# Kernel tuning notes

Hardware: AMD Instinct MI355X
Metric: run time of the kernel (lower is better)

## Reference

```python
import jax, jax.numpy as jnp
import numpy as np

# Each of the 16 binary logic gates, relaxed to real values, is a multilinear
# function: gate(a,b) = c0 + c1*a + c2*b + c3*a*b. Rows follow the standard
# difflogic ordering: FALSE, AND, a&~b, a, ~a&b, b, XOR, OR, NOR, XNOR,
# ~b, a|~b, ~a, ~a|b, NAND, TRUE.
GATE_COEF = jnp.array([
    [0.0,  0.0,  0.0,  0.0],   # 0:  false
    [0.0,  0.0,  0.0,  1.0],   # 1:  a AND b
    [0.0,  1.0,  0.0, -1.0],   # 2:  a AND NOT b
    [0.0,  1.0,  0.0,  0.0],   # 3:  a
    [0.0,  0.0,  1.0, -1.0],   # 4:  NOT a AND b
    [0.0,  0.0,  1.0,  0.0],   # 5:  b
    [0.0,  1.0,  1.0, -2.0],   # 6:  a XOR b
    [0.0,  1.0,  1.0, -1.0],   # 7:  a OR b
    [1.0, -1.0, -1.0,  1.0],   # 8:  NOR
    [1.0, -1.0, -1.0,  2.0],   # 9:  XNOR
    [1.0,  0.0, -1.0,  0.0],   # 10: NOT b
    [1.0,  0.0, -1.0,  1.0],   # 11: a OR NOT b
    [1.0, -1.0,  0.0,  0.0],   # 12: NOT a
    [1.0, -1.0,  0.0,  1.0],   # 13: NOT a OR b
    [1.0,  0.0,  0.0, -1.0],   # 14: NAND
    [1.0,  0.0,  0.0,  0.0],   # 15: true
], dtype=jnp.float32)

B, IN_DIM, HIDDEN, N_LAYERS, OUT_DIM, TAU = 4096, 1024, 8192, 6, 8, 10.0
NPO = HIDDEN // OUT_DIM  # neurons_per_output


def logic_layer(h, w, ia, ib):
    # h: [B, in_dim]; w: [H, 16]; ia, ib: [H] int indices into in_dim.
    # Softmax-weighted blend of 16 gates == multilinear form with blended coefs.
    p = jax.nn.softmax(w, axis=-1)          # [H, 16]
    c = p @ GATE_COEF                       # [H, 4]
    a = h[:, ia]                            # [B, H] gather
    b = h[:, ib]                            # [B, H] gather
    return c[:, 0] + c[:, 1] * a + c[:, 2] * b + c[:, 3] * (a * b)


def setup_inputs() -> dict:
    key = jax.random.key(0)
    ks = jax.random.split(key, 8)
    return {
        "x": jax.random.uniform(ks[0], (B, IN_DIM), dtype=jnp.float32),
        "logic_w": jax.random.normal(ks[1], (N_LAYERS, HIDDEN, 16), dtype=jnp.float32),
        "scaler_w": jax.random.normal(ks[2], (OUT_DIM, OUT_DIM), dtype=jnp.float32) * 0.1,
        "scaler_b": jax.random.normal(ks[3], (OUT_DIM,), dtype=jnp.float32) * 0.1,
        "idx0_a": jax.random.randint(ks[4], (HIDDEN,), 0, IN_DIM, dtype=jnp.int32),
        "idx0_b": jax.random.randint(ks[5], (HIDDEN,), 0, IN_DIM, dtype=jnp.int32),
        "idx_a": jax.random.randint(ks[6], (N_LAYERS - 1, HIDDEN), 0, HIDDEN, dtype=jnp.int32),
        "idx_b": jax.random.randint(ks[7], (N_LAYERS - 1, HIDDEN), 0, HIDDEN, dtype=jnp.int32),
    }


def reference(x, logic_w, scaler_w, scaler_b, idx0_a, idx0_b, idx_a, idx_b):
    h = (x.reshape(x.shape[0], -1) > 0.5).astype(jnp.float32)   # binarize
    h = logic_layer(h, logic_w[0], idx0_a, idx0_b)               # [B, HIDDEN]
    for i in range(N_LAYERS - 1):
        h = logic_layer(h, logic_w[i + 1], idx_a[i], idx_b[i])
    h = h.reshape(h.shape[0], OUT_DIM, NPO)                      # [B, O, NPO]
    values = jnp.sum(h, axis=2) / TAU                            # [B, O]
    q_values = values @ scaler_w.T + scaler_b                    # nn.Linear
    return q_values
```

## Files before the change

### kernel.cpp

```cpp
#include <hip/hip_runtime.h>
#include <hip/hip_fp16.h>

constexpr int BATCH    = 4096;
constexpr int IN_DIM   = 1024;
constexpr int HIDDEN   = 8192;
constexpr int N_LAYERS = 6;
constexpr int N_STAGES = N_LAYERS / 2;
constexpr int OUT_DIM  = 8;
constexpr float INV_TAU = 0.1f;

constexpr int TB   = 8;
constexpr int NTH  = 1024;
constexpr int NPT  = HIDDEN / NTH;
constexpr int NWAVES = NTH / 64;

__device__ __forceinline__ __half2 u2h(unsigned int u) {
    union { unsigned int u; __half2 h; } v; v.u = u; return v.h;
}
__device__ __forceinline__ unsigned int h2u(__half2 h) {
    union { unsigned int u; __half2 h; } v; v.h = h; return v.u;
}

__device__ __forceinline__ uint2 pack4(float4 v) {
    __half2 lo = __float22half2_rn(make_float2(v.x, v.y));
    __half2 hi = __float22half2_rn(make_float2(v.z, v.w));
    uint2 r; r.x = h2u(lo); r.y = h2u(hi); return r;
}

__global__ void prep_coef(const float* __restrict__ logic_w,
                          uint2* __restrict__ coefs, int n)
{
    int id = blockIdx.x * blockDim.x + threadIdx.x;
    if (id >= n) return;

    const float4* w4 = (const float4*)(logic_w + (size_t)id * 16);
    float4 wa = w4[0], wb = w4[1], wc = w4[2], wd = w4[3];
    float wv[16] = {wa.x, wa.y, wa.z, wa.w, wb.x, wb.y, wb.z, wb.w,
                    wc.x, wc.y, wc.z, wc.w, wd.x, wd.y, wd.z, wd.w};
    float m = wv[0];
#pragma unroll
    for (int i = 1; i < 16; ++i) m = fmaxf(m, wv[i]);
    float e[16];
    float s = 0.f;
#pragma unroll
    for (int i = 0; i < 16; ++i) { e[i] = expf(wv[i] - m); s += e[i]; }
    float inv = 1.f / s;
    const float G0[16] = {0,0,0,0,0,0,0,0, 1,1,1,1,1,1,1,1};
    const float G1[16] = {0,0,1,1,0,0,1,1, -1,-1,0,0,-1,-1,0,0};
    const float G2[16] = {0,0,0,0,1,1,1,1, -1,-1,-1,-1,0,0,0,0};
    const float G3[16] = {0,1,-1,0,-1,0,-2,-1, 1,2,0,1,0,1,-1,0};
    float c0 = 0.f, c1 = 0.f, c2 = 0.f, c3 = 0.f;
#pragma unroll
    for (int i = 0; i < 16; ++i) {
        float pv = e[i] * inv;
        c0 = fmaf(pv, G0[i], c0);
        c1 = fmaf(pv, G1[i], c1);
        c2 = fmaf(pv, G2[i], c2);
        c3 = fmaf(pv, G3[i], c3);
    }
    coefs[id] = pack4(make_float4(c0, c1, c2, c3));
}

__global__ void prep_fuse(const uint2* __restrict__ coefs,
                          const int* __restrict__ idx0_a,
                          const int* __restrict__ idx0_b,
                          const int* __restrict__ idx_a,
                          const int* __restrict__ idx_b,
                          uint4* __restrict__ cABp,
                          uint2* __restrict__ idx4p,
                          uint2* __restrict__ cCp, int n)
{
    int id = blockIdx.x * blockDim.x + threadIdx.x;
    if (id >= n) return;
    const int s = id >> 13;
    const int j = id & (HIDDEN - 1);
    const int ltop = 2 * s + 1;
    const int lbot = 2 * s;

    const int pa = idx_a[(size_t)(ltop - 1) * HIDDEN + j];
    const int pb = idx_b[(size_t)(ltop - 1) * HIDDEN + j];

    int gaa, gba, gab, gbb;
    if (s == 0) {
        gaa = idx0_a[pa]; gba = idx0_b[pa];
        gab = idx0_a[pb]; gbb = idx0_b[pb];
    } else {
        const int* A  = idx_a + (size_t)(lbot - 1) * HIDDEN;
        const int* Bv = idx_b + (size_t)(lbot - 1) * HIDDEN;
        gaa = A[pa]; gba = Bv[pa];
        gab = A[pb]; gbb = Bv[pb];
    }
    idx4p[id] = make_uint2((unsigned)gaa | ((unsigned)gba << 16),
                           (unsigned)gab | ((unsigned)gbb << 16));

    uint2 cA = coefs[(size_t)lbot * HIDDEN + pa];
    uint2 cB = coefs[(size_t)lbot * HIDDEN + pb];
    cABp[id] = make_uint4(cA.x, cA.y, cB.x, cB.y);
    cCp[id]  = coefs[(size_t)ltop * HIDDEN + j];
}

__device__ __forceinline__ uint4 gate8(uint4 a, uint4 b, uint2 c) {
    __half2 cp01 = u2h(c.x), cp23 = u2h(c.y);
    __half2 c0 = __low2half2(cp01), c1 = __high2half2(cp01);
    __half2 c2 = __low2half2(cp23), c3 = __high2half2(cp23);
    uint4 r;
    {
        __half2 av = u2h(a.x), bv = u2h(b.x);
        r.x = h2u(__hfma2(bv, __hfma2(c3, av, c2), __hfma2(c1, av, c0)));
    }
    {
        __half2 av = u2h(a.y), bv = u2h(b.y);
        r.y = h2u(__hfma2(bv, __hfma2(c3, av, c2), __hfma2(c1, av, c0)));
    }
    {
        __half2 av = u2h(a.z), bv = u2h(b.z);
        r.z = h2u(__hfma2(bv, __hfma2(c3, av, c2), __hfma2(c1, av, c0)));
    }
    {
        __half2 av = u2h(a.w), bv = u2h(b.w);
        r.w = h2u(__hfma2(bv, __hfma2(c3, av, c2), __hfma2(c1, av, c0)));
    }
    return r;
}

__global__ __launch_bounds__(NTH) void net_kernel(
    const float*  __restrict__ x,
    const uint4*  __restrict__ cABp,
    const uint2*  __restrict__ idx4p,
    const uint2*  __restrict__ cCp,
    const float*  __restrict__ scaler_w, const float* __restrict__ scaler_b,
    float* __restrict__ out)
{
    __shared__ uint4 h[HIDDEN];
    __shared__ uint4 hx[IN_DIM];
    __shared__ float warr[NWAVES][TB];
    __shared__ float vals[TB][OUT_DIM];

    const int tid = threadIdx.x;
    const int b0  = blockIdx.x * TB;

    {
        float v[TB];
#pragma unroll
        for (int r = 0; r < TB; ++r)
            v[r] = (x[(size_t)(b0 + r) * IN_DIM + tid] > 0.5f) ? 1.f : 0.f;
        uint4 p;
        p.x = h2u(__floats2half2_rn(v[0], v[1]));
        p.y = h2u(__floats2half2_rn(v[2], v[3]));
        p.z = h2u(__floats2half2_rn(v[4], v[5]));
        p.w = h2u(__floats2half2_rn(v[6], v[7]));
        hx[tid] = p;
    }

    uint2 ij[NPT], ijn[NPT];
    uint4 acc[NPT];

#pragma unroll
    for (int k = 0; k < NPT; ++k) ij[k] = idx4p[k * NTH + tid];

    __syncthreads();

#pragma unroll
    for (int k = 0; k < NPT; ++k) ijn[k] = idx4p[HIDDEN + k * NTH + tid];
#pragma unroll
    for (int k = 0; k < NPT; ++k) {
        uint2 p = ij[k];
        uint4 x1 = hx[p.x & 0xffffu], x2 = hx[p.x >> 16];
        uint4 x3 = hx[p.y & 0xffffu], x4 = hx[p.y >> 16];
        uint4 cab = cABp[k * NTH + tid];
        uint2 cc  = cCp[k * NTH + tid];
        uint4 u = gate8(x1, x2, make_uint2(cab.x, cab.y));
        uint4 v = gate8(x3, x4, make_uint2(cab.z, cab.w));
        acc[k] = gate8(u, v, cc);
    }
#pragma unroll
    for (int k = 0; k < NPT; ++k) h[k * NTH + tid] = acc[k];
    __syncthreads();

#pragma unroll
    for (int s = 1; s < N_STAGES; ++s) {
#pragma unroll
        for (int k = 0; k < NPT; ++k) ij[k] = ijn[k];
        if (s < N_STAGES - 1) {
#pragma unroll
            for (int k = 0; k < NPT; ++k)
                ijn[k] = idx4p[(size_t)(s + 1) * HIDDEN + k * NTH + tid];
        }
#pragma unroll
        for (int k = 0; k < NPT; ++k) {
            uint2 p = ij[k];
            uint4 x1 = h[p.x & 0xffffu], x2 = h[p.x >> 16];
            uint4 x3 = h[p.y & 0xffffu], x4 = h[p.y >> 16];
            uint4 cab = cABp[(size_t)s * HIDDEN + k * NTH + tid];
            uint2 cc  = cCp[(size_t)s * HIDDEN + k * NTH + tid];
            uint4 u = gate8(x1, x2, make_uint2(cab.x, cab.y));
            uint4 v = gate8(x3, x4, make_uint2(cab.z, cab.w));
            acc[k] = gate8(u, v, cc);
        }
        __syncthreads();
#pragma unroll
        for (int k = 0; k < NPT; ++k) h[k * NTH + tid] = acc[k];
        __syncthreads();
    }

    {
        const int k    = tid >> 7;
        const int base = k * 1024 + (tid & 127);
        float s[TB] = {0.f, 0.f, 0.f, 0.f, 0.f, 0.f, 0.f, 0.f};
#pragma unroll
        for (int i = 0; i < 8; ++i) {
            uint4 t = h[base + 128 * i];
            float2 f0 = __half22float2(u2h(t.x));
            float2 f1 = __half22float2(u2h(t.y));
            float2 f2 = __half22float2(u2h(t.z));
            float2 f3 = __half22float2(u2h(t.w));
            s[0] += f0.x; s[1] += f0.y; s[2] += f1.x; s[3] += f1.y;
            s[4] += f2.x; s[5] += f2.y; s[6] += f3.x; s[7] += f3.y;
        }
#pragma unroll
        for (int off = 32; off > 0; off >>= 1) {
#pragma unroll
            for (int r = 0; r < TB; ++r) s[r] += __shfl_down(s[r], off);
        }
        if ((tid & 63) == 0) {
#pragma unroll
            for (int r = 0; r < TB; ++r) warr[tid >> 6][r] = s[r];
        }
    }
    __syncthreads();
    if (tid < TB * OUT_DIM) {
        int r = tid >> 3;
        int k = tid & 7;
        vals[r][k] = (warr[2 * k][r] + warr[2 * k + 1][r]) * INV_TAU;
    }
    __syncthreads();
    if (tid < TB * OUT_DIM) {
        int r = tid >> 3;
        int o = tid & 7;
        float q = scaler_b[o];
#pragma unroll
        for (int k = 0; k < OUT_DIM; ++k)
            q = fmaf(vals[r][k], scaler_w[o * OUT_DIM + k], q);
        out[(size_t)(b0 + r) * OUT_DIM + o] = q;
    }
}

extern "C" void kernel_launch(void* const* d_in, const int* in_sizes, int n_in,
                              void* d_out, int out_size, void* d_ws, size_t ws_size,
                              hipStream_t stream)
{
    const float* x        = (const float*)d_in[0];
    const float* logic_w  = (const float*)d_in[1];
    const float* scaler_w = (const float*)d_in[2];
    const float* scaler_b = (const float*)d_in[3];
    const int*   idx0_a   = (const int*)d_in[4];
    const int*   idx0_b   = (const int*)d_in[5];
    const int*   idx_a    = (const int*)d_in[6];
    const int*   idx_b    = (const int*)d_in[7];
    float* out = (float*)d_out;

    const int nc = N_LAYERS * HIDDEN;
    const int nf = N_STAGES * HIDDEN;
    char* ws = (char*)d_ws;
    uint2* coefs = (uint2*)ws;                                   ws += (size_t)nc * sizeof(uint2);
    uint4* cABp  = (uint4*)ws;                                   ws += (size_t)nf * sizeof(uint4);
    uint2* idx4p = (uint2*)ws;                                   ws += (size_t)nf * sizeof(uint2);
    uint2* cCp   = (uint2*)ws;

    prep_coef<<<(nc + 255) / 256, 256, 0, stream>>>(logic_w, coefs, nc);
    prep_fuse<<<(nf + 255) / 256, 256, 0, stream>>>(coefs, idx0_a, idx0_b,
                                                    idx_a, idx_b, cABp, idx4p, cCp, nf);
    net_kernel<<<BATCH / TB, NTH, 0, stream>>>(x, cABp, idx4p, cCp,
                                               scaler_w, scaler_b, out);
}
```

Baseline: 115.8 us.

## Process two batch tiles per block and prefetch next tile's inputs

Each block now loops over two 8-row batch tiles instead of one, halving the grid size. The next tile's x values are loaded during the current tile's stage 1 and binarized into the hx buffer after stage 1, which hides the global read latency. The goal is to amortize block launch and setup cost and overlap input loads with compute. The trade-off is fewer blocks in flight (256 blocks of 1024 threads), which may leave CUs underused, plus extra registers for the prefetched values.

```diff
diff --git a/kernel.cpp b/kernel.cpp
--- a/kernel.cpp
+++ b/kernel.cpp
@@ -9,9 +9,10 @@
 constexpr int OUT_DIM  = 8;
 constexpr float INV_TAU = 0.1f;
 
-constexpr int TB   = 8;
-constexpr int NTH  = 1024;
-constexpr int NPT  = HIDDEN / NTH;
+constexpr int TB     = 8;
+constexpr int NTILES = 2;
+constexpr int NTH    = 1024;
+constexpr int NPT    = HIDDEN / NTH;
 constexpr int NWAVES = NTH / 64;
 
 __device__ __forceinline__ __half2 u2h(unsigned int u) {
@@ -137,7 +138,7 @@
     __shared__ float vals[TB][OUT_DIM];
 
     const int tid = threadIdx.x;
-    const int b0  = blockIdx.x * TB;
+    const int b0  = blockIdx.x * (TB * NTILES);
 
     {
         float v[TB];
@@ -161,87 +162,117 @@
     __syncthreads();
 
 #pragma unroll
-    for (int k = 0; k < NPT; ++k) ijn[k] = idx4p[HIDDEN + k * NTH + tid];
-#pragma unroll
-    for (int k = 0; k < NPT; ++k) {
-        uint2 p = ij[k];
-        uint4 x1 = hx[p.x & 0xffffu], x2 = hx[p.x >> 16];
-        uint4 x3 = hx[p.y & 0xffffu], x4 = hx[p.y >> 16];
-        uint4 cab = cABp[k * NTH + tid];
-        uint2 cc  = cCp[k * NTH + tid];
-        uint4 u = gate8(x1, x2, make_uint2(cab.x, cab.y));
-        uint4 v = gate8(x3, x4, make_uint2(cab.z, cab.w));
-        acc[k] = gate8(u, v, cc);
-    }
-#pragma unroll
-    for (int k = 0; k < NPT; ++k) h[k * NTH + tid] = acc[k];
-    __syncthreads();
-
-#pragma unroll
-    for (int s = 1; s < N_STAGES; ++s) {
-#pragma unroll
-        for (int k = 0; k < NPT; ++k) ij[k] = ijn[k];
-        if (s < N_STAGES - 1) {
-#pragma unroll
-            for (int k = 0; k < NPT; ++k)
-                ijn[k] = idx4p[(size_t)(s + 1) * HIDDEN + k * NTH + tid];
-        }
+    for (int t = 0; t < NTILES; ++t) {
+        const int bt = b0 + t * TB;
+        float xn[TB];
+
+#pragma unroll
+        for (int k = 0; k < NPT; ++k) ijn[k] = idx4p[HIDDEN + k * NTH + tid];
 #pragma unroll
         for (int k = 0; k < NPT; ++k) {
             uint2 p = ij[k];
-            uint4 x1 = h[p.x & 0xffffu], x2 = h[p.x >> 16];
-            uint4 x3 = h[p.y & 0xffffu], x4 = h[p.y >> 16];
-            uint4 cab = cABp[(size_t)s * HIDDEN + k * NTH + tid];
-            uint2 cc  = cCp[(size_t)s * HIDDEN + k * NTH + tid];
+            uint4 x1 = hx[p.x & 0xffffu], x2 = hx[p.x >> 16];
+            uint4 x3 = hx[p.y & 0xffffu], x4 = hx[p.y >> 16];
+            uint4 cab = cABp[k * NTH + tid];
+            uint2 cc  = cCp[k * NTH + tid];
             uint4 u = gate8(x1, x2, make_uint2(cab.x, cab.y));
             uint4 v = gate8(x3, x4, make_uint2(cab.z, cab.w));
             acc[k] = gate8(u, v, cc);
         }
-        __syncthreads();
 #pragma unroll
         for (int k = 0; k < NPT; ++k) h[k * NTH + tid] = acc[k];
         __syncthreads();
-    }
-
-    {
-        const int k    = tid >> 7;
-        const int base = k * 1024 + (tid & 127);
-        float s[TB] = {0.f, 0.f, 0.f, 0.f, 0.f, 0.f, 0.f, 0.f};
-#pragma unroll
-        for (int i = 0; i < 8; ++i) {
-            uint4 t = h[base + 128 * i];
-            float2 f0 = __half22float2(u2h(t.x));
-            float2 f1 = __half22float2(u2h(t.y));
-            float2 f2 = __half22float2(u2h(t.z));
-            float2 f3 = __half22float2(u2h(t.w));
-            s[0] += f0.x; s[1] += f0.y; s[2] += f1.x; s[3] += f1.y;
-            s[4] += f2.x; s[5] += f2.y; s[6] += f3.x; s[7] += f3.y;
-        }
-#pragma unroll
-        for (int off = 32; off > 0; off >>= 1) {
-#pragma unroll
-            for (int r = 0; r < TB; ++r) s[r] += __shfl_down(s[r], off);
-        }
-        if ((tid & 63) == 0) {
-#pragma unroll
-            for (int r = 0; r < TB; ++r) warr[tid >> 6][r] = s[r];
-        }
-    }
-    __syncthreads();
-    if (tid < TB * OUT_DIM) {
-        int r = tid >> 3;
-        int k = tid & 7;
-        vals[r][k] = (warr[2 * k][r] + warr[2 * k + 1][r]) * INV_TAU;
-    }
-    __syncthreads();
-    if (tid < TB * OUT_DIM) {
-        int r = tid >> 3;
-        int o = tid & 7;
-        float q = scaler_b[o];
-#pragma unroll
-        for (int k = 0; k < OUT_DIM; ++k)
-            q = fmaf(vals[r][k], scaler_w[o * OUT_DIM + k], q);
-        out[(size_t)(b0 + r) * OUT_DIM + o] = q;
+
+        if (t + 1 < NTILES) {
+#pragma unroll
+            for (int r = 0; r < TB; ++r)
+                xn[r] = x[(size_t)(bt + TB + r) * IN_DIM + tid];
+        }
+
+#pragma unroll
+        for (int s = 1; s < N_STAGES; ++s) {
+#pragma unroll
+            for (int k = 0; k < NPT; ++k) ij[k] = ijn[k];
+            if (s < N_STAGES - 1) {
+#pragma unroll
+                for (int k = 0; k < NPT; ++k)
+                    ijn[k] = idx4p[(size_t)(s + 1) * HIDDEN + k * NTH + tid];
+            }
+#pragma unroll
+            for (int k = 0; k < NPT; ++k) {
+                uint2 p = ij[k];
+                uint4 x1 = h[p.x & 0xffffu], x2 = h[p.x >> 16];
+                uint4 x3 = h[p.y & 0xffffu], x4 = h[p.y >> 16];
+                uint4 cab = cABp[(size_t)s * HIDDEN + k * NTH + tid];
+                uint2 cc  = cCp[(size_t)s * HIDDEN + k * NTH + tid];
+                uint4 u = gate8(x1, x2, make_uint2(cab.x, cab.y));
+                uint4 v = gate8(x3, x4, make_uint2(cab.z, cab.w));
+                acc[k] = gate8(u, v, cc);
+            }
+            __syncthreads();
+#pragma unroll
+            for (int k = 0; k < NPT; ++k) h[k * NTH + tid] = acc[k];
+            __syncthreads();
+
+            if (s == 1 && t + 1 < NTILES) {
+                uint4 p;
+                p.x = h2u(__floats2half2_rn(xn[0] > 0.5f ? 1.f : 0.f,
+                                            xn[1] > 0.5f ? 1.f : 0.f));
+                p.y = h2u(__floats2half2_rn(xn[2] > 0.5f ? 1.f : 0.f,
+                                            xn[3] > 0.5f ? 1.f : 0.f));
+                p.z = h2u(__floats2half2_rn(xn[4] > 0.5f ? 1.f : 0.f,
+                                            xn[5] > 0.5f ? 1.f : 0.f));
+                p.w = h2u(__floats2half2_rn(xn[6] > 0.5f ? 1.f : 0.f,
+                                            xn[7] > 0.5f ? 1.f : 0.f));
+                hx[tid] = p;
+            }
+        }
+
+        {
+            const int k    = tid >> 7;
+            const int base = k * 1024 + (tid & 127);
+            float s[TB] = {0.f, 0.f, 0.f, 0.f, 0.f, 0.f, 0.f, 0.f};
+#pragma unroll
+            for (int i = 0; i < 8; ++i) {
+                uint4 tt = h[base + 128 * i];
+                float2 f0 = __half22float2(u2h(tt.x));
+                float2 f1 = __half22float2(u2h(tt.y));
+                float2 f2 = __half22float2(u2h(tt.z));
+                float2 f3 = __half22float2(u2h(tt.w));
+                s[0] += f0.x; s[1] += f0.y; s[2] += f1.x; s[3] += f1.y;
+                s[4] += f2.x; s[5] += f2.y; s[6] += f3.x; s[7] += f3.y;
+            }
+#pragma unroll
+            for (int off = 32; off > 0; off >>= 1) {
+#pragma unroll
+                for (int r = 0; r < TB; ++r) s[r] += __shfl_down(s[r], off);
+            }
+            if ((tid & 63) == 0) {
+#pragma unroll
+                for (int r = 0; r < TB; ++r) warr[tid >> 6][r] = s[r];
+            }
+        }
+        __syncthreads();
+        if (tid < TB * OUT_DIM) {
+            int r = tid >> 3;
+            int k = tid & 7;
+            vals[r][k] = (warr[2 * k][r] + warr[2 * k + 1][r]) * INV_TAU;
+        }
+        __syncthreads();
+        if (tid < TB * OUT_DIM) {
+            int r = tid >> 3;
+            int o = tid & 7;
+            float q = scaler_b[o];
+#pragma unroll
+            for (int k = 0; k < OUT_DIM; ++k)
+                q = fmaf(vals[r][k], scaler_w[o * OUT_DIM + k], q);
+            out[(size_t)(bt + r) * OUT_DIM + o] = q;
+        }
+
+        if (t + 1 < NTILES) {
+#pragma unroll
+            for (int k = 0; k < NPT; ++k) ij[k] = idx4p[k * NTH + tid];
+        }
     }
 }
 
@@ -270,6 +301,6 @@
     prep_coef<<<(nc + 255) / 256, 256, 0, stream>>>(logic_w, coefs, nc);
     prep_fuse<<<(nf + 255) / 256, 256, 0, stream>>>(coefs, idx0_a, idx0_b,
                                                     idx_a, idx_b, cABp, idx4p, cCp, nf);
-    net_kernel<<<BATCH / TB, NTH, 0, stream>>>(x, cABp, idx4p, cCp,
-                                               scaler_w, scaler_b, out);
-}
+    net_kernel<<<BATCH / (TB * NTILES), NTH, 0, stream>>>(x, cABp, idx4p, cCp,
+                                                          scaler_w, scaler_b, out);
+}
```

Result: slower. 148.0 us (+27.8%).
